# Kernel optimization log

Measured on AMD Instinct MI355X. Metric: run time of the kernel, lower is better.

Reference implementation:

```python
import math
import jax, jax.numpy as jnp
import numpy as np

B, Q, K, D = 32, 1024, 1024, 128
MASK_VALUE = -1000000.0


def setup_inputs() -> dict:
    key = jax.random.key(0)
    kq, kk, kv, kl = jax.random.split(key, 4)
    return {
        "queries": jax.random.normal(kq, (B, Q, D), dtype=jnp.float32),
        "keys": jax.random.normal(kk, (B, K, D), dtype=jnp.float32),
        "values": jax.random.normal(kv, (B, K, D), dtype=jnp.float32),
        "valid_lens": jax.random.randint(kl, (B,), 1, K + 1, dtype=jnp.int32),
    }


def reference(queries, keys, values, valid_lens):
    d = queries.shape[-1]
    # scores: [B, Q, K]
    scores = jnp.einsum("bqd,bkd->bqk", queries, keys) / math.sqrt(d)
    # key-padding mask: position k valid iff k < valid_lens[b] (broadcast over queries)
    mask = jnp.arange(keys.shape[1])[None, None, :] < valid_lens[:, None, None]
    scores = jnp.where(mask, scores, MASK_VALUE)
    attn = jax.nn.softmax(scores, axis=-1)
    # dropout p=0.0 -> identity
    return jnp.einsum("bqk,bkv->bqv", attn, values)
```

## Files before the change

kernel.cpp:

```cpp
#include <hip/hip_runtime.h>
#include <math.h>

typedef _Float16 f16;
typedef __attribute__((ext_vector_type(8))) _Float16 f16x8;
typedef __attribute__((ext_vector_type(4))) _Float16 f16x4;
typedef __attribute__((ext_vector_type(4))) float f32x4;

constexpr int BATCH = 32;
constexpr int QL = 1024;
constexpr int KL = 1024;
constexpr int D = 128;
constexpr int BQ = 64;
constexpr int BK = 64;
constexpr int DKP = 136;
constexpr int BKP = 72;

#define CSC 0.12752863187087177f

__global__ __launch_bounds__(256, 2)
void attn_fwd(const float* __restrict__ Qp, const float* __restrict__ Kp,
              const float* __restrict__ Vp, const int* __restrict__ VLp,
              float* __restrict__ Op) {
  __shared__ f16 sK[2][BK][DKP];
  __shared__ f16 sVT[2][D][BKP];
  __shared__ f16 sP[4][16][BKP];

  const int tid  = threadIdx.x;
  const int wave = tid >> 6, lane = tid & 63;
  const int l16  = lane & 15, quad = lane >> 4;

  const int id = blockIdx.x;
  const int b  = (((id >> 3) & 3) << 3) | (id & 7);
  const int qt = id >> 5;
  const int vl = VLp[b];

  const float* Kb = Kp + (size_t)b * KL * D;
  const float* Vb = Vp + (size_t)b * KL * D;
  const int ntiles = (vl + BK - 1) / BK;

  const int kf_row[8] = {
    (tid + 0*256) >> 5, (tid + 1*256) >> 5, (tid + 2*256) >> 5, (tid + 3*256) >> 5,
    (tid + 4*256) >> 5, (tid + 5*256) >> 5, (tid + 6*256) >> 5, (tid + 7*256) >> 5 };
  const int kf_c4 = tid & 31;

  float4 kreg[8], vreg[8];

  {
    const float4* Kt = (const float4*)Kb;
    #pragma unroll
    for (int i = 0; i < 8; ++i) kreg[i] = Kt[tid + i * 256];
    #pragma unroll
    for (int i = 0; i < 2; ++i) {
      int f = tid + i * 256;
      const float* base = Vb + (size_t)((f & 15) * 4) * D + (f >> 4) * 4;
      vreg[i * 4 + 0] = *(const float4*)(base);
      vreg[i * 4 + 1] = *(const float4*)(base + D);
      vreg[i * 4 + 2] = *(const float4*)(base + 2 * D);
      vreg[i * 4 + 3] = *(const float4*)(base + 3 * D);
    }
  }

  const float* Qb = Qp + ((size_t)(b * QL + qt * BQ + wave * 16 + l16)) * D;
  f16x8 qfrag[4];
  #pragma unroll
  for (int kc = 0; kc < 4; ++kc) {
    const float* p = Qb + kc * 32 + quad * 8;
    float4 u = *(const float4*)p;
    float4 v = *(const float4*)(p + 4);
    f16x8 f;
    f[0] = (f16)u.x; f[1] = (f16)u.y; f[2] = (f16)u.z; f[3] = (f16)u.w;
    f[4] = (f16)v.x; f[5] = (f16)v.y; f[6] = (f16)v.z; f[7] = (f16)v.w;
    qfrag[kc] = f;
  }

  float m2[4]   = {-INFINITY, -INFINITY, -INFINITY, -INFINITY};
  float lsum[4] = {0.f, 0.f, 0.f, 0.f};
  f32x4 o[8];
  #pragma unroll
  for (int dt = 0; dt < 8; ++dt) o[dt] = (f32x4){0.f, 0.f, 0.f, 0.f};

  #pragma unroll
  for (int i = 0; i < 8; ++i) {
    int row = kf_row[i];
    int rp = (row & 3) * 16 + (row >> 2);
    float4 u = kreg[i];
    f16x4 h;
    h[0] = (f16)u.x; h[1] = (f16)u.y; h[2] = (f16)u.z; h[3] = (f16)u.w;
    *(f16x4*)&sK[0][rp][kf_c4 * 4] = h;
  }
  #pragma unroll
  for (int i = 0; i < 2; ++i) {
    int f = tid + i * 256;
    int k0 = (f & 15) * 4, d0 = (f >> 4) * 4;
    float4 r0 = vreg[i * 4 + 0], r1 = vreg[i * 4 + 1];
    float4 r2 = vreg[i * 4 + 2], r3 = vreg[i * 4 + 3];
    f16x4 h;
    h[0] = (f16)r0.x; h[1] = (f16)r1.x; h[2] = (f16)r2.x; h[3] = (f16)r3.x;
    *(f16x4*)&sVT[0][d0 + 0][k0] = h;
    h[0] = (f16)r0.y; h[1] = (f16)r1.y; h[2] = (f16)r2.y; h[3] = (f16)r3.y;
    *(f16x4*)&sVT[0][d0 + 1][k0] = h;
    h[0] = (f16)r0.z; h[1] = (f16)r1.z; h[2] = (f16)r2.z; h[3] = (f16)r3.z;
    *(f16x4*)&sVT[0][d0 + 2][k0] = h;
    h[0] = (f16)r0.w; h[1] = (f16)r1.w; h[2] = (f16)r2.w; h[3] = (f16)r3.w;
    *(f16x4*)&sVT[0][d0 + 3][k0] = h;
  }
  __syncthreads();

  for (int t = 0; t < ntiles; ++t) {
    const int cur = t & 1, nxt = cur ^ 1;
    const bool more = (t + 1 < ntiles);

    if (more) {
      const float4* Kt = (const float4*)(Kb + (size_t)(t + 1) * BK * D);
      #pragma unroll
      for (int i = 0; i < 8; ++i) kreg[i] = Kt[tid + i * 256];
      const float* Vt = Vb + (size_t)(t + 1) * BK * D;
      #pragma unroll
      for (int i = 0; i < 2; ++i) {
        int f = tid + i * 256;
        const float* base = Vt + (size_t)((f & 15) * 4) * D + (f >> 4) * 4;
        vreg[i * 4 + 0] = *(const float4*)(base);
        vreg[i * 4 + 1] = *(const float4*)(base + D);
        vreg[i * 4 + 2] = *(const float4*)(base + 2 * D);
        vreg[i * 4 + 3] = *(const float4*)(base + 3 * D);
      }
    }

    f32x4 s[4];
    #pragma unroll
    for (int ct = 0; ct < 4; ++ct) {
      f32x4 c = (f32x4){0.f, 0.f, 0.f, 0.f};
      #pragma unroll
      for (int kc = 0; kc < 4; ++kc) {
        f16x8 kf = *(const f16x8*)&sK[cur][ct * 16 + l16][kc * 32 + quad * 8];
        c = __builtin_amdgcn_mfma_f32_16x16x32_f16(qfrag[kc], kf, c, 0, 0, 0);
      }
      s[ct] = c;
    }

    #pragma unroll
    for (int ct = 0; ct < 4; ++ct) {
      bool ok = (t * BK + l16 * 4 + ct) < vl;
      #pragma unroll
      for (int r = 0; r < 4; ++r)
        s[ct][r] = ok ? s[ct][r] * CSC : -1.0e9f;
    }

    float mnew[4], alpha[4], ls[4];
    #pragma unroll
    for (int r = 0; r < 4; ++r) {
      float v = fmaxf(fmaxf(s[0][r], s[1][r]), fmaxf(s[2][r], s[3][r]));
      v = fmaxf(v, __shfl_xor(v, 1));
      v = fmaxf(v, __shfl_xor(v, 2));
      v = fmaxf(v, __shfl_xor(v, 4));
      v = fmaxf(v, __shfl_xor(v, 8));
      mnew[r]  = fmaxf(m2[r], v);
      alpha[r] = __builtin_amdgcn_exp2f(m2[r] - mnew[r]);
      m2[r]    = mnew[r];
      ls[r]    = 0.f;
    }
    #pragma unroll
    for (int ct = 0; ct < 4; ++ct)
      #pragma unroll
      for (int r = 0; r < 4; ++r) {
        float p = __builtin_amdgcn_exp2f(s[ct][r] - mnew[r]);
        s[ct][r] = p;
        ls[r] += p;
      }
    #pragma unroll
    for (int r = 0; r < 4; ++r) {
      float v = ls[r];
      v += __shfl_xor(v, 1);
      v += __shfl_xor(v, 2);
      v += __shfl_xor(v, 4);
      v += __shfl_xor(v, 8);
      lsum[r] = lsum[r] * alpha[r] + v;
    }

    #pragma unroll
    for (int r = 0; r < 4; ++r) {
      f16x4 h;
      h[0] = (f16)s[0][r]; h[1] = (f16)s[1][r];
      h[2] = (f16)s[2][r]; h[3] = (f16)s[3][r];
      *(f16x4*)&sP[wave][quad * 4 + r][l16 * 4] = h;
    }
    #pragma unroll
    for (int dt = 0; dt < 8; ++dt)
      #pragma unroll
      for (int r = 0; r < 4; ++r)
        o[dt][r] *= alpha[r];

    asm volatile("s_waitcnt lgkmcnt(0)" ::: "memory");

    #pragma unroll
    for (int ks = 0; ks < 2; ++ks) {
      f16x8 pf = *(const f16x8*)&sP[wave][l16][ks * 32 + quad * 8];
      #pragma unroll
      for (int dt = 0; dt < 8; ++dt) {
        f16x8 vf = *(const f16x8*)&sVT[cur][dt * 16 + l16][ks * 32 + quad * 8];
        o[dt] = __builtin_amdgcn_mfma_f32_16x16x32_f16(pf, vf, o[dt], 0, 0, 0);
      }
    }

    if (more) {
      #pragma unroll
      for (int i = 0; i < 8; ++i) {
        int row = kf_row[i];
        int rp = (row & 3) * 16 + (row >> 2);
        float4 u = kreg[i];
        f16x4 h;
        h[0] = (f16)u.x; h[1] = (f16)u.y; h[2] = (f16)u.z; h[3] = (f16)u.w;
        *(f16x4*)&sK[nxt][rp][kf_c4 * 4] = h;
      }
      #pragma unroll
      for (int i = 0; i < 2; ++i) {
        int f = tid + i * 256;
        int k0 = (f & 15) * 4, d0 = (f >> 4) * 4;
        float4 r0 = vreg[i * 4 + 0], r1 = vreg[i * 4 + 1];
        float4 r2 = vreg[i * 4 + 2], r3 = vreg[i * 4 + 3];
        f16x4 h;
        h[0] = (f16)r0.x; h[1] = (f16)r1.x; h[2] = (f16)r2.x; h[3] = (f16)r3.x;
        *(f16x4*)&sVT[nxt][d0 + 0][k0] = h;
        h[0] = (f16)r0.y; h[1] = (f16)r1.y; h[2] = (f16)r2.y; h[3] = (f16)r3.y;
        *(f16x4*)&sVT[nxt][d0 + 1][k0] = h;
        h[0] = (f16)r0.z; h[1] = (f16)r1.z; h[2] = (f16)r2.z; h[3] = (f16)r3.z;
        *(f16x4*)&sVT[nxt][d0 + 2][k0] = h;
        h[0] = (f16)r0.w; h[1] = (f16)r1.w; h[2] = (f16)r2.w; h[3] = (f16)r3.w;
        *(f16x4*)&sVT[nxt][d0 + 3][k0] = h;
      }
    }
    __syncthreads();
  }

  float* Ob = Op + ((size_t)(b * QL + qt * BQ + wave * 16)) * D;
  #pragma unroll
  for (int r = 0; r < 4; ++r) {
    float inv = 1.0f / lsum[r];
    int row = quad * 4 + r;
    #pragma unroll
    for (int dt = 0; dt < 8; ++dt)
      Ob[(size_t)row * D + dt * 16 + l16] = o[dt][r] * inv;
  }
}

extern "C" void kernel_launch(void* const* d_in, const int* in_sizes, int n_in,
                              void* d_out, int out_size, void* d_ws, size_t ws_size,
                              hipStream_t stream) {
  const float* Qp = (const float*)d_in[0];
  const float* Kp = (const float*)d_in[1];
  const float* Vp = (const float*)d_in[2];
  const int*   VL = (const int*)d_in[3];
  float* Op = (float*)d_out;

  attn_fwd<<<dim3(QL / BQ * BATCH), dim3(256), 0, stream>>>(Qp, Kp, Vp, VL, Op);
}
```

Baseline: 130.0 us.

## Use packed f16 conversion, DPP reductions, wider K stores, and rotated batch mapping

Replaces scalar float-to-half conversions with packed round-toward-zero conversions and swaps the shuffle-based row max/sum reductions for DPP row operations. K tiles are now loaded as two float4s per thread and written to shared memory as 16-byte stores instead of 8-byte ones. The softmax epilogue is reorganised per row, and the block-to-batch mapping rotates with the query tile to balance uneven valid lengths across the grid. The aim is fewer ALU instructions, cheaper cross-lane reductions and better load balance. The cost is that round-toward-zero changes numerics slightly, and the DPP row controls must reproduce the xor-shuffle pattern within each group of 16 lanes.

```diff
diff --git a/kernel.cpp b/kernel.cpp
--- a/kernel.cpp
+++ b/kernel.cpp
@@ -17,6 +17,43 @@
 
 #define CSC 0.12752863187087177f
 
+static __device__ __forceinline__ f16x4 pk4(float x, float y, float z, float w) {
+  auto a = __builtin_amdgcn_cvt_pkrtz(x, y);
+  auto b = __builtin_amdgcn_cvt_pkrtz(z, w);
+  f16x4 h;
+  h[0] = (f16)a[0]; h[1] = (f16)a[1]; h[2] = (f16)b[0]; h[3] = (f16)b[1];
+  return h;
+}
+static __device__ __forceinline__ f16x8 pk8(float4 u, float4 v) {
+  f16x4 a = pk4(u.x, u.y, u.z, u.w);
+  f16x4 b = pk4(v.x, v.y, v.z, v.w);
+  f16x8 h;
+  h[0] = a[0]; h[1] = a[1]; h[2] = a[2]; h[3] = a[3];
+  h[4] = b[0]; h[5] = b[1]; h[6] = b[2]; h[7] = b[3];
+  return h;
+}
+
+template <int CTRL>
+static __device__ __forceinline__ float dppf(float v) {
+  int x = __float_as_int(v);
+  x = __builtin_amdgcn_update_dpp(x, x, CTRL, 0xf, 0xf, false);
+  return __int_as_float(x);
+}
+static __device__ __forceinline__ float rmax16(float v) {
+  v = fmaxf(v, dppf<0xB1>(v));
+  v = fmaxf(v, dppf<0x4E>(v));
+  v = fmaxf(v, dppf<0x141>(v));
+  v = fmaxf(v, dppf<0x140>(v));
+  return v;
+}
+static __device__ __forceinline__ float rsum16(float v) {
+  v += dppf<0xB1>(v);
+  v += dppf<0x4E>(v);
+  v += dppf<0x141>(v);
+  v += dppf<0x140>(v);
+  return v;
+}
+
 __global__ __launch_bounds__(256, 2)
 void attn_fwd(const float* __restrict__ Qp, const float* __restrict__ Kp,
               const float* __restrict__ Vp, const int* __restrict__ VLp,
@@ -30,25 +67,25 @@
   const int l16  = lane & 15, quad = lane >> 4;
 
   const int id = blockIdx.x;
-  const int b  = (((id >> 3) & 3) << 3) | (id & 7);
   const int qt = id >> 5;
+  const int b  = (id & 7) | (((((id >> 3) & 3) + (qt >> 2)) & 3) << 3);
   const int vl = VLp[b];
 
   const float* Kb = Kp + (size_t)b * KL * D;
   const float* Vb = Vp + (size_t)b * KL * D;
   const int ntiles = (vl + BK - 1) / BK;
 
-  const int kf_row[8] = {
-    (tid + 0*256) >> 5, (tid + 1*256) >> 5, (tid + 2*256) >> 5, (tid + 3*256) >> 5,
-    (tid + 4*256) >> 5, (tid + 5*256) >> 5, (tid + 6*256) >> 5, (tid + 7*256) >> 5 };
-  const int kf_c4 = tid & 31;
-
   float4 kreg[8], vreg[8];
 
   {
     const float4* Kt = (const float4*)Kb;
     #pragma unroll
-    for (int i = 0; i < 8; ++i) kreg[i] = Kt[tid + i * 256];
+    for (int i = 0; i < 4; ++i) {
+      int c = tid + i * 256;
+      int row = c >> 4, d04 = (c & 15) * 2;
+      kreg[2 * i]     = Kt[row * 32 + d04];
+      kreg[2 * i + 1] = Kt[row * 32 + d04 + 1];
+    }
     #pragma unroll
     for (int i = 0; i < 2; ++i) {
       int f = tid + i * 256;
@@ -65,12 +102,7 @@
   #pragma unroll
   for (int kc = 0; kc < 4; ++kc) {
     const float* p = Qb + kc * 32 + quad * 8;
-    float4 u = *(const float4*)p;
-    float4 v = *(const float4*)(p + 4);
-    f16x8 f;
-    f[0] = (f16)u.x; f[1] = (f16)u.y; f[2] = (f16)u.z; f[3] = (f16)u.w;
-    f[4] = (f16)v.x; f[5] = (f16)v.y; f[6] = (f16)v.z; f[7] = (f16)v.w;
-    qfrag[kc] = f;
+    qfrag[kc] = pk8(*(const float4*)p, *(const float4*)(p + 4));
   }
 
   float m2[4]   = {-INFINITY, -INFINITY, -INFINITY, -INFINITY};
@@ -80,29 +112,21 @@
   for (int dt = 0; dt < 8; ++dt) o[dt] = (f32x4){0.f, 0.f, 0.f, 0.f};
 
   #pragma unroll
-  for (int i = 0; i < 8; ++i) {
-    int row = kf_row[i];
+  for (int i = 0; i < 4; ++i) {
+    int c = tid + i * 256;
+    int row = c >> 4, d0 = (c & 15) * 8;
     int rp = (row & 3) * 16 + (row >> 2);
-    float4 u = kreg[i];
-    f16x4 h;
-    h[0] = (f16)u.x; h[1] = (f16)u.y; h[2] = (f16)u.z; h[3] = (f16)u.w;
-    *(f16x4*)&sK[0][rp][kf_c4 * 4] = h;
+    *(f16x8*)&sK[0][rp][d0] = pk8(kreg[2 * i], kreg[2 * i + 1]);
   }
   #pragma unroll
   for (int i = 0; i < 2; ++i) {
     int f = tid + i * 256;
     int k0 = (f & 15) * 4, d0 = (f >> 4) * 4;
-    float4 r0 = vreg[i * 4 + 0], r1 = vreg[i * 4 + 1];
-    float4 r2 = vreg[i * 4 + 2], r3 = vreg[i * 4 + 3];
-    f16x4 h;
-    h[0] = (f16)r0.x; h[1] = (f16)r1.x; h[2] = (f16)r2.x; h[3] = (f16)r3.x;
-    *(f16x4*)&sVT[0][d0 + 0][k0] = h;
-    h[0] = (f16)r0.y; h[1] = (f16)r1.y; h[2] = (f16)r2.y; h[3] = (f16)r3.y;
-    *(f16x4*)&sVT[0][d0 + 1][k0] = h;
-    h[0] = (f16)r0.z; h[1] = (f16)r1.z; h[2] = (f16)r2.z; h[3] = (f16)r3.z;
-    *(f16x4*)&sVT[0][d0 + 2][k0] = h;
-    h[0] = (f16)r0.w; h[1] = (f16)r1.w; h[2] = (f16)r2.w; h[3] = (f16)r3.w;
-    *(f16x4*)&sVT[0][d0 + 3][k0] = h;
+    float4 r0 = vreg[i*4+0], r1 = vreg[i*4+1], r2 = vreg[i*4+2], r3 = vreg[i*4+3];
+    *(f16x4*)&sVT[0][d0 + 0][k0] = pk4(r0.x, r1.x, r2.x, r3.x);
+    *(f16x4*)&sVT[0][d0 + 1][k0] = pk4(r0.y, r1.y, r2.y, r3.y);
+    *(f16x4*)&sVT[0][d0 + 2][k0] = pk4(r0.z, r1.z, r2.z, r3.z);
+    *(f16x4*)&sVT[0][d0 + 3][k0] = pk4(r0.w, r1.w, r2.w, r3.w);
   }
   __syncthreads();
 
@@ -113,7 +137,12 @@
     if (more) {
       const float4* Kt = (const float4*)(Kb + (size_t)(t + 1) * BK * D);
       #pragma unroll
-      for (int i = 0; i < 8; ++i) kreg[i] = Kt[tid + i * 256];
+      for (int i = 0; i < 4; ++i) {
+        int c = tid + i * 256;
+        int row = c >> 4, d04 = (c & 15) * 2;
+        kreg[2 * i]     = Kt[row * 32 + d04];
+        kreg[2 * i + 1] = Kt[row * 32 + d04 + 1];
+      }
       const float* Vt = Vb + (size_t)(t + 1) * BK * D;
       #pragma unroll
       for (int i = 0; i < 2; ++i) {
@@ -146,49 +175,30 @@
         s[ct][r] = ok ? s[ct][r] * CSC : -1.0e9f;
     }
 
-    float mnew[4], alpha[4], ls[4];
+    float mnew[4], alpha[4];
     #pragma unroll
     for (int r = 0; r < 4; ++r) {
       float v = fmaxf(fmaxf(s[0][r], s[1][r]), fmaxf(s[2][r], s[3][r]));
-      v = fmaxf(v, __shfl_xor(v, 1));
-      v = fmaxf(v, __shfl_xor(v, 2));
-      v = fmaxf(v, __shfl_xor(v, 4));
-      v = fmaxf(v, __shfl_xor(v, 8));
+      v = rmax16(v);
       mnew[r]  = fmaxf(m2[r], v);
       alpha[r] = __builtin_amdgcn_exp2f(m2[r] - mnew[r]);
       m2[r]    = mnew[r];
-      ls[r]    = 0.f;
-    }
-    #pragma unroll
-    for (int ct = 0; ct < 4; ++ct)
-      #pragma unroll
-      for (int r = 0; r < 4; ++r) {
+    }
+    #pragma unroll
+    for (int r = 0; r < 4; ++r) {
+      float ls = 0.f;
+      #pragma unroll
+      for (int ct = 0; ct < 4; ++ct) {
         float p = __builtin_amdgcn_exp2f(s[ct][r] - mnew[r]);
         s[ct][r] = p;
-        ls[r] += p;
-      }
-    #pragma unroll
-    for (int r = 0; r < 4; ++r) {
-      float v = ls[r];
-      v += __shfl_xor(v, 1);
-      v += __shfl_xor(v, 2);
-      v += __shfl_xor(v, 4);
-      v += __shfl_xor(v, 8);
-      lsum[r] = lsum[r] * alpha[r] + v;
-    }
-
-    #pragma unroll
-    for (int r = 0; r < 4; ++r) {
-      f16x4 h;
-      h[0] = (f16)s[0][r]; h[1] = (f16)s[1][r];
-      h[2] = (f16)s[2][r]; h[3] = (f16)s[3][r];
-      *(f16x4*)&sP[wave][quad * 4 + r][l16 * 4] = h;
-    }
-    #pragma unroll
-    for (int dt = 0; dt < 8; ++dt)
-      #pragma unroll
-      for (int r = 0; r < 4; ++r)
-        o[dt][r] *= alpha[r];
+        ls += p;
+      }
+      lsum[r] = lsum[r] * alpha[r] + rsum16(ls);
+      *(f16x4*)&sP[wave][quad * 4 + r][l16 * 4] =
+          pk4(s[0][r], s[1][r], s[2][r], s[3][r]);
+      #pragma unroll
+      for (int dt = 0; dt < 8; ++dt) o[dt][r] *= alpha[r];
+    }
 
     asm volatile("s_waitcnt lgkmcnt(0)" ::: "memory");
 
@@ -204,29 +214,21 @@
 
     if (more) {
       #pragma unroll
-      for (int i = 0; i < 8; ++i) {
-        int row = kf_row[i];
+      for (int i = 0; i < 4; ++i) {
+        int c = tid + i * 256;
+        int row = c >> 4, d0 = (c & 15) * 8;
         int rp = (row & 3) * 16 + (row >> 2);
-        float4 u = kreg[i];
-        f16x4 h;
-        h[0] = (f16)u.x; h[1] = (f16)u.y; h[2] = (f16)u.z; h[3] = (f16)u.w;
-        *(f16x4*)&sK[nxt][rp][kf_c4 * 4] = h;
+        *(f16x8*)&sK[nxt][rp][d0] = pk8(kreg[2 * i], kreg[2 * i + 1]);
       }
       #pragma unroll
       for (int i = 0; i < 2; ++i) {
         int f = tid + i * 256;
         int k0 = (f & 15) * 4, d0 = (f >> 4) * 4;
-        float4 r0 = vreg[i * 4 + 0], r1 = vreg[i * 4 + 1];
-        float4 r2 = vreg[i * 4 + 2], r3 = vreg[i * 4 + 3];
-        f16x4 h;
-        h[0] = (f16)r0.x; h[1] = (f16)r1.x; h[2] = (f16)r2.x; h[3] = (f16)r3.x;
-        *(f16x4*)&sVT[nxt][d0 + 0][k0] = h;
-        h[0] = (f16)r0.y; h[1] = (f16)r1.y; h[2] = (f16)r2.y; h[3] = (f16)r3.y;
-        *(f16x4*)&sVT[nxt][d0 + 1][k0] = h;
-        h[0] = (f16)r0.z; h[1] = (f16)r1.z; h[2] = (f16)r2.z; h[3] = (f16)r3.z;
-        *(f16x4*)&sVT[nxt][d0 + 2][k0] = h;
-        h[0] = (f16)r0.w; h[1] = (f16)r1.w; h[2] = (f16)r2.w; h[3] = (f16)r3.w;
-        *(f16x4*)&sVT[nxt][d0 + 3][k0] = h;
+        float4 r0 = vreg[i*4+0], r1 = vreg[i*4+1], r2 = vreg[i*4+2], r3 = vreg[i*4+3];
+        *(f16x4*)&sVT[nxt][d0 + 0][k0] = pk4(r0.x, r1.x, r2.x, r3.x);
+        *(f16x4*)&sVT[nxt][d0 + 1][k0] = pk4(r0.y, r1.y, r2.y, r3.y);
+        *(f16x4*)&sVT[nxt][d0 + 2][k0] = pk4(r0.z, r1.z, r2.z, r3.z);
+        *(f16x4*)&sVT[nxt][d0 + 3][k0] = pk4(r0.w, r1.w, r2.w, r3.w);
       }
     }
     __syncthreads();
```

After: 120.8 us. 1.08x faster.
